# Kernel optimization log

Measured on AMD Instinct MI355X. Metric: run time of the kernel, lower is better.

Reference implementation:

```python
import jax, jax.numpy as jnp
import numpy as np

DEPTH = 4
EPS = 1e-5


def block_pool(x, g):
    # adaptive max pool over a g x g grid of blocks, broadcast back to full size.
    # Equivalent to the recursive HalfSplit/adaptive_max_pool2d/QuarterStitch pyramid.
    B, C, H, W = x.shape
    xr = x.reshape(B, C, g, H // g, g, W // g)
    m = xr.max(axis=(3, 5), keepdims=True)          # [B,C,g,1,g,1]
    return jnp.broadcast_to(m, xr.shape).reshape(B, C, H, W)


def conv1x1_bn(x, w, gamma, beta):
    # Conv2DNormed: 1x1 conv (no bias) followed by BatchNorm (batch statistics).
    y = jnp.einsum('bchw,oc->bohw', x, w)
    mu = y.mean(axis=(0, 2, 3), keepdims=True)
    var = y.var(axis=(0, 2, 3), keepdims=True)
    yhat = (y - mu) * jax.lax.rsqrt(var + EPS)
    return yhat * gamma[None, :, None, None] + beta[None, :, None, None]


def setup_inputs() -> dict:
    key = jax.random.key(0)
    k0, k1, k2 = jax.random.split(key, 3)
    B, C, H, W = 4, 256, 192, 192
    x = jax.random.normal(k0, (B, C, H, W), jnp.float32)
    ws = jax.random.normal(k1, (DEPTH, C, C), jnp.float32) / np.float32(np.sqrt(C))
    gs = jnp.ones((DEPTH, C), jnp.float32)
    bs = jnp.zeros((DEPTH, C), jnp.float32)
    wf = jax.random.normal(k2, (C, (DEPTH + 1) * C), jnp.float32) / np.float32(np.sqrt((DEPTH + 1) * C))
    gf = jnp.ones((C,), jnp.float32)
    bf = jnp.zeros((C,), jnp.float32)
    return {"x": x, "ws": ws, "gs": gs, "bs": bs, "wf": wf, "gf": gf, "bf": bf}


def reference(x, ws, gs, bs, wf, gf, bf):
    # p[0] = raw input; p[1+d] = conv_d(block-pooled input at grid 2^d), d=0..DEPTH-1
    p = [x]
    for d in range(DEPTH):
        pooled = block_pool(x, 2 ** d)
        p.append(conv1x1_bn(pooled, ws[d], gs[d], bs[d]))
    out = jnp.concatenate(p, axis=1)                # [B, (DEPTH+1)*C, H, W]
    return conv1x1_bn(out, wf, gf, bf)
```

## Files before the change

### kernel.cpp

```cpp
#include <hip/hip_runtime.h>

typedef unsigned short u16;
typedef unsigned int   u32;
typedef __attribute__((ext_vector_type(4))) float f32x4;
typedef __attribute__((ext_vector_type(8))) short s16x8;
typedef __attribute__((ext_vector_type(4))) unsigned short u16x4;
typedef __attribute__((ext_vector_type(8))) unsigned short u16x8;

#define HW    36864
#define NCH   256
#define NB    4
#define NPIX  147456
#define POS   85
#define BN_EPS 1e-5f
#define NBKT  16

#define WS_PALL    0
#define WS_YD      87040
#define WS_PSUM    174080
#define WS_PSQ     175104
#define WS_CONTRIB 176128
#define WS_FSUMB   241664
#define WS_FSQB    245760
#define WS_WPK     249856
#define WS_YBF     282624
#define WS_TOT1    (WS_YBF + NB*NCH*HW/2)

__device__ __forceinline__ u16 f2bf(float f) {
  u32 u = __builtin_bit_cast(u32, f);
  u += 0x7fffu + ((u >> 16) & 1u);
  return (u16)(u >> 16);
}
__device__ __forceinline__ float bf2f(u16 h) {
  u32 u = ((u32)h) << 16;
  return __builtin_bit_cast(float, u);
}

__global__ __launch_bounds__(192) void k_pool(const float* __restrict__ x, float* __restrict__ wsb) {
  __shared__ float sm[8][4][48];
  __shared__ float sp[84];
  int bc = blockIdx.x;
  const float* base = x + (size_t)bc * HW;
  int t = threadIdx.x;
  int cg = t % 48, rg = t / 48;
  if (bc == 0) {
    for (int i = t; i < 2048; i += 192) wsb[WS_PSUM + i] = 0.f;
    for (int i = t; i < 8192; i += 192) wsb[WS_FSUMB + i] = 0.f;
  }
  #pragma unroll
  for (int byi = 0; byi < 8; byi++) {
    float mm = -3.4e38f;
    #pragma unroll
    for (int rr = 0; rr < 6; rr++) {
      int r = byi*24 + rg + 4*rr;
      f32x4 v = *(const f32x4*)(base + r*192 + cg*4);
      mm = fmaxf(mm, fmaxf(fmaxf(v.x, v.y), fmaxf(v.z, v.w)));
    }
    sm[byi][rg][cg] = mm;
  }
  __syncthreads();
  size_t pb = WS_PALL + (size_t)bc * POS;
  if (t < 64) {
    int by = t >> 3, bx = t & 7;
    float mm = -3.4e38f;
    for (int r2 = 0; r2 < 4; r2++)
      for (int cq = 0; cq < 6; cq++)
        mm = fmaxf(mm, sm[by][r2][bx*6 + cq]);
    sp[t] = mm;
    wsb[pb + t] = mm;
  }
  __syncthreads();
  if (t < 16) {
    int i = t >> 2, j = t & 3;
    float mm = fmaxf(fmaxf(sp[(2*i)*8 + 2*j], sp[(2*i)*8 + 2*j + 1]),
                     fmaxf(sp[(2*i+1)*8 + 2*j], sp[(2*i+1)*8 + 2*j + 1]));
    sp[64 + t] = mm;
    wsb[pb + 64 + t] = mm;
  }
  __syncthreads();
  if (t < 4) {
    int i = t >> 1, j = t & 1;
    float mm = fmaxf(fmaxf(sp[64 + (2*i)*4 + 2*j], sp[64 + (2*i)*4 + 2*j + 1]),
                     fmaxf(sp[64 + (2*i+1)*4 + 2*j], sp[64 + (2*i+1)*4 + 2*j + 1]));
    sp[80 + t] = mm;
    wsb[pb + 80 + t] = mm;
  }
  __syncthreads();
  if (t == 0)
    wsb[pb + 84] = fmaxf(fmaxf(sp[80], sp[81]), fmaxf(sp[82], sp[83]));
}

__global__ __launch_bounds__(256) void k_wpack(const float* __restrict__ wf, float* __restrict__ wsb) {
  int fid = blockIdx.x*256 + threadIdx.x;
  int m = fid & 255, g = (fid >> 8) & 3, ks = fid >> 10;
  const float* src = wf + (size_t)m*1280 + ks*32 + g*8;
  f32x4 a = *(const f32x4*)src;
  f32x4 c = *(const f32x4*)(src + 4);
  u32* dst = (u32*)((u16*)(wsb + WS_WPK) + (size_t)fid*8);
  dst[0] = (u32)f2bf(a.x) | ((u32)f2bf(a.y) << 16);
  dst[1] = (u32)f2bf(a.z) | ((u32)f2bf(a.w) << 16);
  dst[2] = (u32)f2bf(c.x) | ((u32)f2bf(c.y) << 16);
  dst[3] = (u32)f2bf(c.z) | ((u32)f2bf(c.w) << 16);
}

__global__ __launch_bounds__(256) void k_pyr(const float* __restrict__ wconv, float* __restrict__ wsb) {
  __shared__ __align__(16) float pv[256];
  int bi = blockIdx.x;
  int b = bi / 85, pos = bi % 85;
  int d = (pos < 64) ? 3 : (pos < 80) ? 2 : (pos < 84) ? 1 : 0;
  int t = threadIdx.x;
  pv[t] = wsb[WS_PALL + (size_t)(b*NCH + t)*POS + pos];
  __syncthreads();
  const float* wrow = wconv + ((size_t)d*NCH + t)*NCH;
  float acc = 0.f;
  #pragma unroll 4
  for (int c4 = 0; c4 < 64; c4++) {
    f32x4 wv = *(const f32x4*)(wrow + c4*4);
    f32x4 xv = *(const f32x4*)(&pv[c4*4]);
    acc += wv.x*xv.x + wv.y*xv.y + wv.z*xv.z + wv.w*xv.w;
  }
  wsb[WS_YD + (size_t)(b*NCH + t)*POS + pos] = acc;
  atomicAdd(&wsb[WS_PSUM + d*NCH + t], acc);
  atomicAdd(&wsb[WS_PSQ  + d*NCH + t], acc*acc);
}

__global__ __launch_bounds__(256) void k_contrib(const float* __restrict__ wf,
                                                 const float* __restrict__ gs,
                                                 const float* __restrict__ bs,
                                                 float* __restrict__ wsb) {
  __shared__ __align__(16) float pn[16][256];
  int cell = blockIdx.x;
  int by = cell >> 3, bx = cell & 7;
  int t = threadIdx.x;
  #pragma unroll
  for (int d = 0; d < 4; d++) {
    int pos = (d == 3) ? cell
            : (d == 2) ? 64 + (by >> 1)*4 + (bx >> 1)
            : (d == 1) ? 80 + (by >> 2)*2 + (bx >> 2)
            : 84;
    float cnt = (float)(4 << (2*d));
    float mu  = wsb[WS_PSUM + d*NCH + t] / cnt;
    float var = wsb[WS_PSQ  + d*NCH + t] / cnt - mu*mu;
    float sc  = gs[d*NCH + t] * rsqrtf(var + BN_EPS);
    float bi_ = bs[d*NCH + t] - mu * sc;
    #pragma unroll
    for (int b = 0; b < 4; b++)
      pn[d*4 + b][t] = wsb[WS_YD + (size_t)(b*NCH + t)*POS + pos] * sc + bi_;
  }
  __syncthreads();
  float a0 = 0.f, a1 = 0.f, a2 = 0.f, a3 = 0.f;
  #pragma unroll
  for (int d = 0; d < 4; d++) {
    const float* wrow = wf + (size_t)t*1280 + 256 + d*256;
    #pragma unroll 4
    for (int j = 0; j < 64; j++) {
      f32x4 wv = *(const f32x4*)(wrow + j*4);
      f32x4 p0 = *(const f32x4*)(&pn[d*4 + 0][j*4]);
      f32x4 p1 = *(const f32x4*)(&pn[d*4 + 1][j*4]);
      f32x4 p2 = *(const f32x4*)(&pn[d*4 + 2][j*4]);
      f32x4 p3 = *(const f32x4*)(&pn[d*4 + 3][j*4]);
      a0 += wv.x*p0.x + wv.y*p0.y + wv.z*p0.z + wv.w*p0.w;
      a1 += wv.x*p1.x + wv.y*p1.y + wv.z*p1.z + wv.w*p1.w;
      a2 += wv.x*p2.x + wv.y*p2.y + wv.z*p2.z + wv.w*p2.w;
      a3 += wv.x*p3.x + wv.y*p3.y + wv.z*p3.z + wv.w*p3.w;
    }
  }
  wsb[WS_CONTRIB + (size_t)(0*NCH + t)*64 + cell] = a0;
  wsb[WS_CONTRIB + (size_t)(1*NCH + t)*64 + cell] = a1;
  wsb[WS_CONTRIB + (size_t)(2*NCH + t)*64 + cell] = a2;
  wsb[WS_CONTRIB + (size_t)(3*NCH + t)*64 + cell] = a3;
}

template<bool YBF>
__global__ __launch_bounds__(256, 3) void k_main(const float* __restrict__ x,
                                                 float* __restrict__ wsb, float* __restrict__ y) {
  __shared__ __align__(16) u32 xbuf[2][64*20];
  __shared__ float ctile[256*4];
  __shared__ __align__(16) u16 ytile[256*72];
  int wg = blockIdx.x;
  int b = wg / 576, tile = wg % 576;
  int n0 = tile * 64;
  int t = threadIdx.x, w = t >> 6, l = t & 63, g = l >> 4, ln = l & 15;
  int cb0 = (tile % 3) * 64;
  int rowblk = (tile / 3) / 24;
  int cblk0 = cb0 / 24;
  const u16* wpk = (const u16*)(wsb + WS_WPK);
  int mrow = w*64 + ln;
  int qq = t & 15, c2 = t >> 4;
  const float* xsrc = x + (size_t)(b*NCH + 2*c2)*HW + n0 + 4*qq;

  float ct[4];
  {
    const float* cbase = wsb + WS_CONTRIB + ((size_t)b*NCH + t)*64 + rowblk*8;
    #pragma unroll
    for (int i = 0; i < 4; i++) {
      int cc = cblk0 + i; if (cc > 7) cc = 7;
      ct[i] = cbase[cc];
    }
  }
  f32x4 xa[4], xbv[4];
  #pragma unroll
  for (int i = 0; i < 4; i++) {
    xa[i]  = *(const f32x4*)(xsrc + (size_t)(i*32)*HW);
    xbv[i] = *(const f32x4*)(xsrc + (size_t)(i*32 + 1)*HW);
  }
  s16x8 af[2][4];
  #pragma unroll
  for (int tm = 0; tm < 4; tm++)
    af[0][tm] = *(const s16x8*)(wpk + ((size_t)g*256 + mrow + tm*16)*8);

  #pragma unroll
  for (int i = 0; i < 4; i++) ctile[t*4 + i] = ct[i];
  asm volatile("s_waitcnt lgkmcnt(0)" ::: "memory");
  __builtin_amdgcn_s_barrier();
  __builtin_amdgcn_sched_barrier(0);

  f32x4 acc[4][4];
  #pragma unroll
  for (int i = 0; i < 4; i++)
    #pragma unroll
    for (int j = 0; j < 4; j++)
      acc[i][j] = {0.f, 0.f, 0.f, 0.f};

  int slot = (((c2 >> 2) ^ (qq & 3)) << 2) | (c2 & 3);

  #pragma unroll
  for (int i = 0; i < 8; i++) {
    {
      u32* dst = &xbuf[i & 1][0];
      f32x4 va = xa[i & 3], vb = xbv[i & 3];
      #pragma unroll
      for (int j = 0; j < 4; j++) {
        u32 pk = (u32)f2bf(va[j]) | ((u32)f2bf(vb[j]) << 16);
        dst[(4*qq + j)*20 + slot] = pk;
      }
    }
    asm volatile("s_waitcnt lgkmcnt(0)" ::: "memory");
    __builtin_amdgcn_s_barrier();
    __builtin_amdgcn_sched_barrier(0);
    if (i < 4) {
      xa[i & 3]  = *(const f32x4*)(xsrc + (size_t)((i+4)*32)*HW);
      xbv[i & 3] = *(const f32x4*)(xsrc + (size_t)((i+4)*32 + 1)*HW);
    }
    if (i < 7) {
      #pragma unroll
      for (int tm = 0; tm < 4; tm++)
        af[(i+1) & 1][tm] = *(const s16x8*)(wpk + ((size_t)((i+1)*4 + g)*256 + mrow + tm*16)*8);
    }
    #pragma unroll
    for (int tn = 0; tn < 4; tn++) {
      int px = 16*tn + ln;
      int gr = g ^ ((px >> 2) & 3);
      s16x8 bfr = *(const s16x8*)((const u16*)&xbuf[i & 1][px*20 + gr*4]);
      #pragma unroll
      for (int tm = 0; tm < 4; tm++)
        acc[tm][tn] = __builtin_amdgcn_mfma_f32_16x16x32_bf16(af[i & 1][tm], bfr, acc[tm][tn], 0, 0, 0);
    }
  }

  int ci[4];
  #pragma unroll
  for (int tn = 0; tn < 4; tn++)
    ci[tn] = (cb0 + 16*tn + ln)/24 - cblk0;
  int bkt = wg & (NBKT - 1);
  float* fsum = wsb + WS_FSUMB + bkt*256;
  float* fsq  = wsb + WS_FSQB  + bkt*256;
  float* yf   = y + (size_t)b*NCH*HW + n0;
  #pragma unroll
  for (int tm = 0; tm < 4; tm++) {
    #pragma unroll
    for (int r = 0; r < 4; r++) {
      int o = w*64 + tm*16 + g*4 + r;
      float s1 = 0.f, s2 = 0.f;
      #pragma unroll
      for (int tn = 0; tn < 4; tn++) {
        int px = 16*tn + ln;
        float v = acc[tm][tn][r] + ctile[o*4 + ci[tn]];
        if (YBF) {
          u16 h = f2bf(v);
          ytile[o*72 + px] = h;
          float yr = bf2f(h);
          s1 += yr; s2 += yr*yr;
        } else {
          yf[(size_t)o*HW + px] = v;
          s1 += v; s2 += v*v;
        }
      }
      s1 += __shfl_xor(s1, 1);  s2 += __shfl_xor(s2, 1);
      s1 += __shfl_xor(s1, 2);  s2 += __shfl_xor(s2, 2);
      s1 += __shfl_xor(s1, 4);  s2 += __shfl_xor(s2, 4);
      s1 += __shfl_xor(s1, 8);  s2 += __shfl_xor(s2, 8);
      if (ln == 0) { atomicAdd(&fsum[o], s1); atomicAdd(&fsq[o], s2); }
    }
  }
  if (YBF) {
    __syncthreads();
    u16* ybb = (u16*)(wsb + WS_YBF) + (size_t)b*NCH*HW + n0;
    int oo = t >> 3, seg = t & 7;
    #pragma unroll
    for (int r8 = 0; r8 < 8; r8++) {
      int o = r8*32 + oo;
      u16x8 v = *(const u16x8*)(&ytile[o*72 + seg*8]);
      *(u16x8*)(ybb + (size_t)o*HW + seg*8) = v;
    }
  }
}

template<bool YBF>
__global__ __launch_bounds__(256) void k_norm(float* __restrict__ out,
                                              const float* __restrict__ gf,
                                              const float* __restrict__ bfv,
                                              const float* __restrict__ wsb) {
  int bid = blockIdx.x;
  int plane = bid >> 2, q = bid & 3;
  int c = plane & 255;
  float s1 = 0.f, s2 = 0.f;
  #pragma unroll
  for (int i = 0; i < NBKT; i++) {
    s1 += wsb[WS_FSUMB + i*256 + c];
    s2 += wsb[WS_FSQB  + i*256 + c];
  }
  float inv = 1.f / (float)NPIX;
  float mu  = s1 * inv;
  float var = s2 * inv - mu*mu;
  float sc  = gf[c] * rsqrtf(var + BN_EPS);
  float bi  = bfv[c] - mu * sc;
  size_t base4 = ((size_t)plane*HW + q*(HW/4)) >> 2;
  int t = threadIdx.x;
  if (YBF) {
    const u16* yb = (const u16*)(wsb + WS_YBF);
    #pragma unroll
    for (int it = 0; it < 9; it++) {
      size_t i4 = base4 + it*256 + t;
      u16x4 v = *(const u16x4*)(yb + i4*4);
      f32x4 o;
      o.x = bf2f(v[0])*sc + bi;
      o.y = bf2f(v[1])*sc + bi;
      o.z = bf2f(v[2])*sc + bi;
      o.w = bf2f(v[3])*sc + bi;
      ((f32x4*)out)[i4] = o;
    }
  } else {
    #pragma unroll
    for (int it = 0; it < 9; it++) {
      size_t i4 = base4 + it*256 + t;
      f32x4 v = ((f32x4*)out)[i4];
      v.x = v.x*sc + bi; v.y = v.y*sc + bi; v.z = v.z*sc + bi; v.w = v.w*sc + bi;
      ((f32x4*)out)[i4] = v;
    }
  }
}

extern "C" void kernel_launch(void* const* d_in, const int* in_sizes, int n_in,
                              void* d_out, int out_size, void* d_ws, size_t ws_size,
                              hipStream_t stream) {
  const float* x  = (const float*)d_in[0];
  const float* w  = (const float*)d_in[1];
  const float* gs = (const float*)d_in[2];
  const float* bs = (const float*)d_in[3];
  const float* wf = (const float*)d_in[4];
  const float* gf = (const float*)d_in[5];
  const float* bf = (const float*)d_in[6];
  float* y   = (float*)d_out;
  float* wsb = (float*)d_ws;

  bool ybf = ws_size >= (size_t)WS_TOT1 * sizeof(float);

  k_pool   <<<NB*NCH, 192, 0, stream>>>(x, wsb);
  k_wpack  <<<32, 256, 0, stream>>>(wf, wsb);
  k_pyr    <<<NB*POS, 256, 0, stream>>>(w, wsb);
  k_contrib<<<64, 256, 0, stream>>>(wf, gs, bs, wsb);
  if (ybf) k_main<true> <<<NB*576, 256, 0, stream>>>(x, wsb, y);
  else     k_main<false><<<NB*576, 256, 0, stream>>>(x, wsb, y);
  if (ybf) k_norm<true> <<<4096, 256, 0, stream>>>(y, gf, bf, wsb);
  else     k_norm<false><<<4096, 256, 0, stream>>>(y, gf, bf, wsb);
}
```

Before: 201.8 us.

## Fuse block max-pool into main GEMM and defer per-cell pyramid contribution

Removes the separate pooling pass over x by computing per-cell maxima inside the main GEMM kernel with LDS and global atomicMax on order-preserving float encodings. The pyramid contribution is no longer added before bf16 rounding. Instead, per-cell sums of y are accumulated and the final BN statistics are reconstructed analytically in a new single-block stats kernel, with the per-cell additive term folded into the normalize pass. This saves one full read of x but adds atomics, a serial single-block reduction kernel, and a small change in numerics.

```diff
diff --git a/kernel.cpp b/kernel.cpp
--- a/kernel.cpp
+++ b/kernel.cpp
@@ -15,15 +15,18 @@
 #define BN_EPS 1e-5f
 #define NBKT  16
 
-#define WS_PALL    0
-#define WS_YD      87040
-#define WS_PSUM    174080
-#define WS_PSQ     175104
-#define WS_CONTRIB 176128
-#define WS_FSUMB   241664
-#define WS_FSQB    245760
-#define WS_WPK     249856
-#define WS_YBF     282624
+#define WS_P3      0
+#define WS_PALL    65536
+#define WS_YD      152576
+#define WS_PSUM    239616
+#define WS_PSQ     240640
+#define WS_CONTRIB 241664
+#define WS_S1      307200
+#define WS_FSQB    372736
+#define WS_SC      376832
+#define WS_ADD     377088
+#define WS_WPK     442624
+#define WS_YBF     475392
 #define WS_TOT1    (WS_YBF + NB*NCH*HW/2)
 
 __device__ __forceinline__ u16 f2bf(float f) {
@@ -35,63 +38,26 @@
   u32 u = ((u32)h) << 16;
   return __builtin_bit_cast(float, u);
 }
-
-__global__ __launch_bounds__(192) void k_pool(const float* __restrict__ x, float* __restrict__ wsb) {
-  __shared__ float sm[8][4][48];
-  __shared__ float sp[84];
-  int bc = blockIdx.x;
-  const float* base = x + (size_t)bc * HW;
-  int t = threadIdx.x;
-  int cg = t % 48, rg = t / 48;
-  if (bc == 0) {
-    for (int i = t; i < 2048; i += 192) wsb[WS_PSUM + i] = 0.f;
-    for (int i = t; i < 8192; i += 192) wsb[WS_FSUMB + i] = 0.f;
-  }
-  #pragma unroll
-  for (int byi = 0; byi < 8; byi++) {
-    float mm = -3.4e38f;
-    #pragma unroll
-    for (int rr = 0; rr < 6; rr++) {
-      int r = byi*24 + rg + 4*rr;
-      f32x4 v = *(const f32x4*)(base + r*192 + cg*4);
-      mm = fmaxf(mm, fmaxf(fmaxf(v.x, v.y), fmaxf(v.z, v.w)));
-    }
-    sm[byi][rg][cg] = mm;
-  }
-  __syncthreads();
-  size_t pb = WS_PALL + (size_t)bc * POS;
-  if (t < 64) {
-    int by = t >> 3, bx = t & 7;
-    float mm = -3.4e38f;
-    for (int r2 = 0; r2 < 4; r2++)
-      for (int cq = 0; cq < 6; cq++)
-        mm = fmaxf(mm, sm[by][r2][bx*6 + cq]);
-    sp[t] = mm;
-    wsb[pb + t] = mm;
-  }
-  __syncthreads();
-  if (t < 16) {
-    int i = t >> 2, j = t & 3;
-    float mm = fmaxf(fmaxf(sp[(2*i)*8 + 2*j], sp[(2*i)*8 + 2*j + 1]),
-                     fmaxf(sp[(2*i+1)*8 + 2*j], sp[(2*i+1)*8 + 2*j + 1]));
-    sp[64 + t] = mm;
-    wsb[pb + 64 + t] = mm;
-  }
-  __syncthreads();
-  if (t < 4) {
-    int i = t >> 1, j = t & 1;
-    float mm = fmaxf(fmaxf(sp[64 + (2*i)*4 + 2*j], sp[64 + (2*i)*4 + 2*j + 1]),
-                     fmaxf(sp[64 + (2*i+1)*4 + 2*j], sp[64 + (2*i+1)*4 + 2*j + 1]));
-    sp[80 + t] = mm;
-    wsb[pb + 80 + t] = mm;
-  }
-  __syncthreads();
-  if (t == 0)
-    wsb[pb + 84] = fmaxf(fmaxf(sp[80], sp[81]), fmaxf(sp[82], sp[83]));
+__device__ __forceinline__ u32 encf(float f) {
+  u32 b = __builtin_bit_cast(u32, f);
+  return (b & 0x80000000u) ? ~b : (b | 0x80000000u);
+}
+__device__ __forceinline__ float decf(u32 k) {
+  u32 b = (k & 0x80000000u) ? (k & 0x7fffffffu) : ~k;
+  return __builtin_bit_cast(float, b);
 }
 
 __global__ __launch_bounds__(256) void k_wpack(const float* __restrict__ wf, float* __restrict__ wsb) {
-  int fid = blockIdx.x*256 + threadIdx.x;
+  int blk = blockIdx.x, t = threadIdx.x;
+  if (blk >= 32) {
+    int id = (blk - 32)*256 + t;
+    wsb[WS_P3 + id] = 0.f;
+    wsb[WS_S1 + id] = 0.f;
+    if (id < 4096) wsb[WS_FSQB + id] = 0.f;
+    if (id < 2048) wsb[WS_PSUM + id] = 0.f;
+    return;
+  }
+  int fid = blk*256 + t;
   int m = fid & 255, g = (fid >> 8) & 3, ks = fid >> 10;
   const float* src = wf + (size_t)m*1280 + ks*32 + g*8;
   f32x4 a = *(const f32x4*)src;
@@ -101,6 +67,216 @@
   dst[1] = (u32)f2bf(a.z) | ((u32)f2bf(a.w) << 16);
   dst[2] = (u32)f2bf(c.x) | ((u32)f2bf(c.y) << 16);
   dst[3] = (u32)f2bf(c.z) | ((u32)f2bf(c.w) << 16);
+}
+
+template<bool YBF>
+__global__ __launch_bounds__(256, 3) void k_main(const float* __restrict__ x,
+                                                 float* __restrict__ wsb, float* __restrict__ y) {
+  __shared__ __align__(16) u32 xbuf[2][64*20];
+  __shared__ u32 pmaxl[256*4];
+  __shared__ __align__(16) u16 ytile[128*72];
+  int wg = blockIdx.x;
+  int b = wg / 576, tile = wg % 576;
+  int n0 = tile * 64;
+  int row = tile / 3;
+  int t = threadIdx.x, w = t >> 6, l = t & 63, g = l >> 4, ln = l & 15;
+  int cb0 = (tile % 3) * 64;
+  int cblk0 = cb0 / 24;
+  int maxcl = (cb0 + 63)/24 - cblk0;
+  int cellbase = (row/24)*8 + cblk0;
+  const u16* wpk = (const u16*)(wsb + WS_WPK);
+  int mrow = w*64 + ln;
+  int qq = t & 15, c2 = t >> 4;
+  int cellLoc = (cb0 + 4*qq)/24 - cblk0;
+  const float* xsrc = x + (size_t)(b*NCH + 2*c2)*HW + n0 + 4*qq;
+
+  #pragma unroll
+  for (int j = 0; j < 4; j++) pmaxl[t*4 + j] = 0u;
+
+  f32x4 xa[4], xbv[4];
+  #pragma unroll
+  for (int i = 0; i < 4; i++) {
+    xa[i]  = *(const f32x4*)(xsrc + (size_t)(i*32)*HW);
+    xbv[i] = *(const f32x4*)(xsrc + (size_t)(i*32 + 1)*HW);
+  }
+  s16x8 af[2][4];
+  #pragma unroll
+  for (int tm = 0; tm < 4; tm++)
+    af[0][tm] = *(const s16x8*)(wpk + ((size_t)g*256 + mrow + tm*16)*8);
+
+  asm volatile("s_waitcnt lgkmcnt(0)" ::: "memory");
+  __builtin_amdgcn_s_barrier();
+  __builtin_amdgcn_sched_barrier(0);
+
+  f32x4 acc[4][4];
+  #pragma unroll
+  for (int i = 0; i < 4; i++)
+    #pragma unroll
+    for (int j = 0; j < 4; j++)
+      acc[i][j] = {0.f, 0.f, 0.f, 0.f};
+
+  int slot = (((c2 >> 2) ^ (qq & 3)) << 2) | (c2 & 3);
+
+  #pragma unroll
+  for (int i = 0; i < 8; i++) {
+    {
+      u32* dst = &xbuf[i & 1][0];
+      f32x4 va = xa[i & 3], vb = xbv[i & 3];
+      #pragma unroll
+      for (int j = 0; j < 4; j++) {
+        u32 pk = (u32)f2bf(va[j]) | ((u32)f2bf(vb[j]) << 16);
+        dst[(4*qq + j)*20 + slot] = pk;
+      }
+      float ma = fmaxf(fmaxf(va.x, va.y), fmaxf(va.z, va.w));
+      float mb = fmaxf(fmaxf(vb.x, vb.y), fmaxf(vb.z, vb.w));
+      int ca = 2*c2 + 32*i;
+      atomicMax(&pmaxl[ca*4 + cellLoc], encf(ma));
+      atomicMax(&pmaxl[(ca + 1)*4 + cellLoc], encf(mb));
+    }
+    asm volatile("s_waitcnt lgkmcnt(0)" ::: "memory");
+    __builtin_amdgcn_s_barrier();
+    __builtin_amdgcn_sched_barrier(0);
+    if (i < 4) {
+      xa[i & 3]  = *(const f32x4*)(xsrc + (size_t)((i+4)*32)*HW);
+      xbv[i & 3] = *(const f32x4*)(xsrc + (size_t)((i+4)*32 + 1)*HW);
+    }
+    if (i < 7) {
+      #pragma unroll
+      for (int tm = 0; tm < 4; tm++)
+        af[(i+1) & 1][tm] = *(const s16x8*)(wpk + ((size_t)((i+1)*4 + g)*256 + mrow + tm*16)*8);
+    }
+    #pragma unroll
+    for (int tn = 0; tn < 4; tn++) {
+      int px = 16*tn + ln;
+      int gr = g ^ ((px >> 2) & 3);
+      s16x8 bfr = *(const s16x8*)((const u16*)&xbuf[i & 1][px*20 + gr*4]);
+      #pragma unroll
+      for (int tm = 0; tm < 4; tm++)
+        acc[tm][tn] = __builtin_amdgcn_mfma_f32_16x16x32_bf16(af[i & 1][tm], bfr, acc[tm][tn], 0, 0, 0);
+    }
+  }
+
+  {
+    u32* P3g = (u32*)(wsb + WS_P3) + ((size_t)(b*NCH + t))*64 + cellbase;
+    #pragma unroll
+    for (int j = 0; j < 4; j++) {
+      if (j <= maxcl) { u32 v = pmaxl[t*4 + j]; if (v) atomicMax(&P3g[j], v); }
+    }
+  }
+
+  int bkt = wg & (NBKT - 1);
+  float* fsqb = wsb + WS_FSQB + bkt*256;
+  float* S1g  = wsb + WS_S1 + ((size_t)b*NCH)*64;
+
+  if (YBF) {
+    u16* ybb = (u16*)(wsb + WS_YBF) + (size_t)b*NCH*HW + n0;
+    #pragma unroll
+    for (int half = 0; half < 2; half++) {
+      if ((w >> 1) == half) {
+        #pragma unroll
+        for (int tm = 0; tm < 4; tm++)
+          #pragma unroll
+          for (int r = 0; r < 4; r++) {
+            int orow = (w & 1)*64 + tm*16 + g*4 + r;
+            #pragma unroll
+            for (int tn = 0; tn < 4; tn++)
+              ytile[orow*72 + 16*tn + ln] = f2bf(acc[tm][tn][r]);
+          }
+      }
+      __syncthreads();
+      int oo = t >> 3, seg = t & 7;
+      int basec = cb0 + seg*8;
+      int loG = basec/24, hiG = (basec + 7)/24;
+      int kk = (loG + 1)*24 - basec; if (kk > 8) kk = 8;
+      int lo = loG - cblk0, hi = hiG - cblk0;
+      #pragma unroll
+      for (int r8 = 0; r8 < 4; r8++) {
+        int ol = r8*32 + oo;
+        int o  = half*128 + ol;
+        u16x8 v = *(const u16x8*)&ytile[ol*72 + seg*8];
+        *(u16x8*)(ybb + (size_t)o*HW + seg*8) = v;
+        float p_lo = 0.f, p_hi = 0.f, s2p = 0.f;
+        #pragma unroll
+        for (int e = 0; e < 8; e++) {
+          float yr = bf2f(v[e]);
+          s2p += yr*yr;
+          if (e < kk) p_lo += yr; else p_hi += yr;
+        }
+        s2p += __shfl_xor(s2p, 1); s2p += __shfl_xor(s2p, 2); s2p += __shfl_xor(s2p, 4);
+        if (seg == 0) atomicAdd(&fsqb[o], s2p);
+        float* S1o = S1g + (size_t)o*64 + cellbase;
+        #pragma unroll
+        for (int cl = 0; cl < 4; cl++) {
+          float val = (lo == cl ? p_lo : 0.f) + (hi == cl ? p_hi : 0.f);
+          val += __shfl_xor(val, 1); val += __shfl_xor(val, 2); val += __shfl_xor(val, 4);
+          if (seg == cl && cl <= maxcl) atomicAdd(&S1o[cl], val);
+        }
+      }
+      __syncthreads();
+    }
+  } else {
+    float* yf = y + (size_t)b*NCH*HW + n0;
+    #pragma unroll
+    for (int tm = 0; tm < 4; tm++) {
+      #pragma unroll
+      for (int r = 0; r < 4; r++) {
+        int o = w*64 + tm*16 + g*4 + r;
+        float s1c0 = 0.f, s1c1 = 0.f, s1c2 = 0.f, s1c3 = 0.f, s2 = 0.f;
+        #pragma unroll
+        for (int tn = 0; tn < 4; tn++) {
+          int px = 16*tn + ln;
+          float v = acc[tm][tn][r];
+          yf[(size_t)o*HW + px] = v;
+          int ci = (cb0 + px)/24 - cblk0;
+          s1c0 += (ci == 0) ? v : 0.f;
+          s1c1 += (ci == 1) ? v : 0.f;
+          s1c2 += (ci == 2) ? v : 0.f;
+          s1c3 += (ci == 3) ? v : 0.f;
+          s2 += v*v;
+        }
+        s2 += __shfl_xor(s2, 1); s2 += __shfl_xor(s2, 2);
+        s2 += __shfl_xor(s2, 4); s2 += __shfl_xor(s2, 8);
+        if (ln == 0) atomicAdd(&fsqb[o], s2);
+        float* S1o = S1g + (size_t)o*64 + cellbase;
+        float sv[4] = {s1c0, s1c1, s1c2, s1c3};
+        #pragma unroll
+        for (int cl = 0; cl < 4; cl++) {
+          float val = sv[cl];
+          val += __shfl_xor(val, 1); val += __shfl_xor(val, 2);
+          val += __shfl_xor(val, 4); val += __shfl_xor(val, 8);
+          if (ln == cl && cl <= maxcl) atomicAdd(&S1o[cl], val);
+        }
+      }
+    }
+  }
+}
+
+__global__ __launch_bounds__(64) void k_ppyr(float* __restrict__ wsb) {
+  __shared__ float sm3[64], sm2[16], sm1[4];
+  int bc = blockIdx.x;
+  int t = threadIdx.x;
+  const u32* p3 = (const u32*)(wsb + WS_P3) + (size_t)bc*64;
+  float leaf = decf(p3[t]);
+  sm3[t] = leaf;
+  __syncthreads();
+  float* pb = wsb + WS_PALL + (size_t)bc*POS;
+  pb[t] = leaf;
+  if (t < 16) {
+    int i = t >> 2, j = t & 3;
+    float m = fmaxf(fmaxf(sm3[(2*i)*8 + 2*j], sm3[(2*i)*8 + 2*j + 1]),
+                    fmaxf(sm3[(2*i+1)*8 + 2*j], sm3[(2*i+1)*8 + 2*j + 1]));
+    sm2[t] = m; pb[64 + t] = m;
+  }
+  __syncthreads();
+  if (t < 4) {
+    int i = t >> 1, j = t & 1;
+    float m = fmaxf(fmaxf(sm2[(2*i)*4 + 2*j], sm2[(2*i)*4 + 2*j + 1]),
+                    fmaxf(sm2[(2*i+1)*4 + 2*j], sm2[(2*i+1)*4 + 2*j + 1]));
+    sm1[t] = m; pb[80 + t] = m;
+  }
+  __syncthreads();
+  if (t == 0)
+    pb[84] = fmaxf(fmaxf(sm1[0], sm1[1]), fmaxf(sm1[2], sm1[3]));
 }
 
 __global__ __launch_bounds__(256) void k_pyr(const float* __restrict__ wconv, float* __restrict__ wsb) {
@@ -171,181 +347,75 @@
   wsb[WS_CONTRIB + (size_t)(3*NCH + t)*64 + cell] = a3;
 }
 
-template<bool YBF>
-__global__ __launch_bounds__(256, 3) void k_main(const float* __restrict__ x,
-                                                 float* __restrict__ wsb, float* __restrict__ y) {
-  __shared__ __align__(16) u32 xbuf[2][64*20];
-  __shared__ float ctile[256*4];
-  __shared__ __align__(16) u16 ytile[256*72];
-  int wg = blockIdx.x;
-  int b = wg / 576, tile = wg % 576;
-  int n0 = tile * 64;
-  int t = threadIdx.x, w = t >> 6, l = t & 63, g = l >> 4, ln = l & 15;
-  int cb0 = (tile % 3) * 64;
-  int rowblk = (tile / 3) / 24;
-  int cblk0 = cb0 / 24;
-  const u16* wpk = (const u16*)(wsb + WS_WPK);
-  int mrow = w*64 + ln;
-  int qq = t & 15, c2 = t >> 4;
-  const float* xsrc = x + (size_t)(b*NCH + 2*c2)*HW + n0 + 4*qq;
-
-  float ct[4];
-  {
-    const float* cbase = wsb + WS_CONTRIB + ((size_t)b*NCH + t)*64 + rowblk*8;
-    #pragma unroll
-    for (int i = 0; i < 4; i++) {
-      int cc = cblk0 + i; if (cc > 7) cc = 7;
-      ct[i] = cbase[cc];
-    }
-  }
-  f32x4 xa[4], xbv[4];
-  #pragma unroll
-  for (int i = 0; i < 4; i++) {
-    xa[i]  = *(const f32x4*)(xsrc + (size_t)(i*32)*HW);
-    xbv[i] = *(const f32x4*)(xsrc + (size_t)(i*32 + 1)*HW);
-  }
-  s16x8 af[2][4];
-  #pragma unroll
-  for (int tm = 0; tm < 4; tm++)
-    af[0][tm] = *(const s16x8*)(wpk + ((size_t)g*256 + mrow + tm*16)*8);
-
-  #pragma unroll
-  for (int i = 0; i < 4; i++) ctile[t*4 + i] = ct[i];
-  asm volatile("s_waitcnt lgkmcnt(0)" ::: "memory");
-  __builtin_amdgcn_s_barrier();
-  __builtin_amdgcn_sched_barrier(0);
-
-  f32x4 acc[4][4];
-  #pragma unroll
-  for (int i = 0; i < 4; i++)
-    #pragma unroll
-    for (int j = 0; j < 4; j++)
-      acc[i][j] = {0.f, 0.f, 0.f, 0.f};
-
-  int slot = (((c2 >> 2) ^ (qq & 3)) << 2) | (c2 & 3);
-
-  #pragma unroll
-  for (int i = 0; i < 8; i++) {
-    {
-      u32* dst = &xbuf[i & 1][0];
-      f32x4 va = xa[i & 3], vb = xbv[i & 3];
-      #pragma unroll
-      for (int j = 0; j < 4; j++) {
-        u32 pk = (u32)f2bf(va[j]) | ((u32)f2bf(vb[j]) << 16);
-        dst[(4*qq + j)*20 + slot] = pk;
-      }
-    }
-    asm volatile("s_waitcnt lgkmcnt(0)" ::: "memory");
-    __builtin_amdgcn_s_barrier();
-    __builtin_amdgcn_sched_barrier(0);
-    if (i < 4) {
-      xa[i & 3]  = *(const f32x4*)(xsrc + (size_t)((i+4)*32)*HW);
-      xbv[i & 3] = *(const f32x4*)(xsrc + (size_t)((i+4)*32 + 1)*HW);
-    }
-    if (i < 7) {
-      #pragma unroll
-      for (int tm = 0; tm < 4; tm++)
-        af[(i+1) & 1][tm] = *(const s16x8*)(wpk + ((size_t)((i+1)*4 + g)*256 + mrow + tm*16)*8);
-    }
-    #pragma unroll
-    for (int tn = 0; tn < 4; tn++) {
-      int px = 16*tn + ln;
-      int gr = g ^ ((px >> 2) & 3);
-      s16x8 bfr = *(const s16x8*)((const u16*)&xbuf[i & 1][px*20 + gr*4]);
-      #pragma unroll
-      for (int tm = 0; tm < 4; tm++)
-        acc[tm][tn] = __builtin_amdgcn_mfma_f32_16x16x32_bf16(af[i & 1][tm], bfr, acc[tm][tn], 0, 0, 0);
-    }
-  }
-
-  int ci[4];
-  #pragma unroll
-  for (int tn = 0; tn < 4; tn++)
-    ci[tn] = (cb0 + 16*tn + ln)/24 - cblk0;
-  int bkt = wg & (NBKT - 1);
-  float* fsum = wsb + WS_FSUMB + bkt*256;
-  float* fsq  = wsb + WS_FSQB  + bkt*256;
-  float* yf   = y + (size_t)b*NCH*HW + n0;
-  #pragma unroll
-  for (int tm = 0; tm < 4; tm++) {
-    #pragma unroll
-    for (int r = 0; r < 4; r++) {
-      int o = w*64 + tm*16 + g*4 + r;
-      float s1 = 0.f, s2 = 0.f;
-      #pragma unroll
-      for (int tn = 0; tn < 4; tn++) {
-        int px = 16*tn + ln;
-        float v = acc[tm][tn][r] + ctile[o*4 + ci[tn]];
-        if (YBF) {
-          u16 h = f2bf(v);
-          ytile[o*72 + px] = h;
-          float yr = bf2f(h);
-          s1 += yr; s2 += yr*yr;
-        } else {
-          yf[(size_t)o*HW + px] = v;
-          s1 += v; s2 += v*v;
-        }
-      }
-      s1 += __shfl_xor(s1, 1);  s2 += __shfl_xor(s2, 1);
-      s1 += __shfl_xor(s1, 2);  s2 += __shfl_xor(s2, 2);
-      s1 += __shfl_xor(s1, 4);  s2 += __shfl_xor(s2, 4);
-      s1 += __shfl_xor(s1, 8);  s2 += __shfl_xor(s2, 8);
-      if (ln == 0) { atomicAdd(&fsum[o], s1); atomicAdd(&fsq[o], s2); }
-    }
-  }
-  if (YBF) {
-    __syncthreads();
-    u16* ybb = (u16*)(wsb + WS_YBF) + (size_t)b*NCH*HW + n0;
-    int oo = t >> 3, seg = t & 7;
-    #pragma unroll
-    for (int r8 = 0; r8 < 8; r8++) {
-      int o = r8*32 + oo;
-      u16x8 v = *(const u16x8*)(&ytile[o*72 + seg*8]);
-      *(u16x8*)(ybb + (size_t)o*HW + seg*8) = v;
-    }
+__global__ __launch_bounds__(256) void k_fstats(const float* __restrict__ gf,
+                                                const float* __restrict__ bfv,
+                                                float* __restrict__ wsb) {
+  int o = threadIdx.x;
+  float sq = 0.f;
+  #pragma unroll
+  for (int i = 0; i < NBKT; i++) sq += wsb[WS_FSQB + i*256 + o];
+  float sum1 = 0.f, sum2 = sq;
+  #pragma unroll 8
+  for (int bc = 0; bc < 256; bc++) {
+    int b = bc >> 6, cell = bc & 63;
+    float s1 = wsb[WS_S1      + ((size_t)(b*NCH + o))*64 + cell];
+    float c  = wsb[WS_CONTRIB + ((size_t)(b*NCH + o))*64 + cell];
+    sum1 += s1 + 576.f*c;
+    sum2 += c*(2.f*s1 + 576.f*c);
+  }
+  float inv = 1.f / (float)NPIX;
+  float mu  = sum1 * inv;
+  float var = sum2 * inv - mu*mu;
+  float sc  = gf[o] * rsqrtf(var + BN_EPS);
+  float bi  = bfv[o] - mu * sc;
+  wsb[WS_SC + o] = sc;
+  #pragma unroll 8
+  for (int bc = 0; bc < 256; bc++) {
+    int b = bc >> 6, cell = bc & 63;
+    float c = wsb[WS_CONTRIB + ((size_t)(b*NCH + o))*64 + cell];
+    wsb[WS_ADD + ((size_t)(b*NCH + o))*64 + cell] = bi + c*sc;
   }
 }
 
 template<bool YBF>
 __global__ __launch_bounds__(256) void k_norm(float* __restrict__ out,
-                                              const float* __restrict__ gf,
-                                              const float* __restrict__ bfv,
                                               const float* __restrict__ wsb) {
+  __shared__ float a16[16];
   int bid = blockIdx.x;
   int plane = bid >> 2, q = bid & 3;
-  int c = plane & 255;
-  float s1 = 0.f, s2 = 0.f;
-  #pragma unroll
-  for (int i = 0; i < NBKT; i++) {
-    s1 += wsb[WS_FSUMB + i*256 + c];
-    s2 += wsb[WS_FSQB  + i*256 + c];
-  }
-  float inv = 1.f / (float)NPIX;
-  float mu  = s1 * inv;
-  float var = s2 * inv - mu*mu;
-  float sc  = gf[c] * rsqrtf(var + BN_EPS);
-  float bi  = bfv[c] - mu * sc;
+  int t = threadIdx.x;
+  float sc = wsb[WS_SC + (plane & 255)];
+  if (t < 16)
+    a16[t] = wsb[WS_ADD + (size_t)plane*64 + (2*q + (t >> 3))*8 + (t & 7)];
+  __syncthreads();
   size_t base4 = ((size_t)plane*HW + q*(HW/4)) >> 2;
-  int t = threadIdx.x;
   if (YBF) {
     const u16* yb = (const u16*)(wsb + WS_YBF);
     #pragma unroll
     for (int it = 0; it < 9; it++) {
+      int pl = 4*(it*256 + t);
+      int rl = pl / 192;
+      int cc = (pl - rl*192) / 24;
+      float ad = a16[(rl/24)*8 + cc];
       size_t i4 = base4 + it*256 + t;
       u16x4 v = *(const u16x4*)(yb + i4*4);
       f32x4 o;
-      o.x = bf2f(v[0])*sc + bi;
-      o.y = bf2f(v[1])*sc + bi;
-      o.z = bf2f(v[2])*sc + bi;
-      o.w = bf2f(v[3])*sc + bi;
+      o.x = bf2f(v[0])*sc + ad;
+      o.y = bf2f(v[1])*sc + ad;
+      o.z = bf2f(v[2])*sc + ad;
+      o.w = bf2f(v[3])*sc + ad;
       ((f32x4*)out)[i4] = o;
     }
   } else {
     #pragma unroll
     for (int it = 0; it < 9; it++) {
+      int pl = 4*(it*256 + t);
+      int rl = pl / 192;
+      int cc = (pl - rl*192) / 24;
+      float ad = a16[(rl/24)*8 + cc];
       size_t i4 = base4 + it*256 + t;
       f32x4 v = ((f32x4*)out)[i4];
-      v.x = v.x*sc + bi; v.y = v.y*sc + bi; v.z = v.z*sc + bi; v.w = v.w*sc + bi;
+      v.x = v.x*sc + ad; v.y = v.y*sc + ad; v.z = v.z*sc + ad; v.w = v.w*sc + ad;
       ((f32x4*)out)[i4] = v;
     }
   }
@@ -366,12 +436,13 @@
 
   bool ybf = ws_size >= (size_t)WS_TOT1 * sizeof(float);
 
-  k_pool   <<<NB*NCH, 192, 0, stream>>>(x, wsb);
-  k_wpack  <<<32, 256, 0, stream>>>(wf, wsb);
+  k_wpack  <<<288, 256, 0, stream>>>(wf, wsb);
+  if (ybf) k_main<true> <<<NB*576, 256, 0, stream>>>(x, wsb, y);
+  else     k_main<false><<<NB*576, 256, 0, stream>>>(x, wsb, y);
+  k_ppyr   <<<NB*NCH, 64, 0, stream>>>(wsb);
   k_pyr    <<<NB*POS, 256, 0, stream>>>(w, wsb);
   k_contrib<<<64, 256, 0, stream>>>(wf, gs, bs, wsb);
-  if (ybf) k_main<true> <<<NB*576, 256, 0, stream>>>(x, wsb, y);
-  else     k_main<false><<<NB*576, 256, 0, stream>>>(x, wsb, y);
-  if (ybf) k_norm<true> <<<4096, 256, 0, stream>>>(y, gf, bf, wsb);
-  else     k_norm<false><<<4096, 256, 0, stream>>>(y, gf, bf, wsb);
-}
+  k_fstats <<<1, 256, 0, stream>>>(gf, bf, wsb);
+  if (ybf) k_norm<true> <<<4096, 256, 0, stream>>>(y, wsb);
+  else     k_norm<false><<<4096, 256, 0, stream>>>(y, wsb);
+}
```

New measurement: 354.2 us. 75.5% more time.

## Fold weight packing into pool kernel and double K-step per barrier in main GEMM

Applied to the files above, without the earlier changes.

Merges the bf16 weight-packing kernel into the pooling kernel as extra blocks, removing one launch. In the main GEMM kernel, each barrier phase now stages two 32-channel K slices into LDS instead of one, which halves the barrier count. The xbuf and ytile buffers now share one LDS allocation, separated by a __syncthreads, to reduce shared memory per block. Weight fragments are loaded just before use instead of being prefetched one step ahead, so their global-load latency may be exposed.

```diff
diff --git a/kernel.cpp b/kernel.cpp
--- a/kernel.cpp
+++ b/kernel.cpp
@@ -36,12 +36,30 @@
   return __builtin_bit_cast(float, u);
 }
 
-__global__ __launch_bounds__(192) void k_pool(const float* __restrict__ x, float* __restrict__ wsb) {
+__global__ __launch_bounds__(192) void k_pool(const float* __restrict__ x,
+                                              const float* __restrict__ wf,
+                                              float* __restrict__ wsb) {
+  int blk = blockIdx.x;
+  int t = threadIdx.x;
+  if (blk >= 1024) {
+    int fid = (blk - 1024)*192 + t;
+    if (fid < 8192) {
+      int m = fid & 255, g = (fid >> 8) & 3, ks = fid >> 10;
+      const float* src = wf + (size_t)m*1280 + ks*32 + g*8;
+      f32x4 a = *(const f32x4*)src;
+      f32x4 c = *(const f32x4*)(src + 4);
+      u32* dst = (u32*)((u16*)(wsb + WS_WPK) + (size_t)fid*8);
+      dst[0] = (u32)f2bf(a.x) | ((u32)f2bf(a.y) << 16);
+      dst[1] = (u32)f2bf(a.z) | ((u32)f2bf(a.w) << 16);
+      dst[2] = (u32)f2bf(c.x) | ((u32)f2bf(c.y) << 16);
+      dst[3] = (u32)f2bf(c.z) | ((u32)f2bf(c.w) << 16);
+    }
+    return;
+  }
   __shared__ float sm[8][4][48];
   __shared__ float sp[84];
-  int bc = blockIdx.x;
+  int bc = blk;
   const float* base = x + (size_t)bc * HW;
-  int t = threadIdx.x;
   int cg = t % 48, rg = t / 48;
   if (bc == 0) {
     for (int i = t; i < 2048; i += 192) wsb[WS_PSUM + i] = 0.f;
@@ -88,19 +106,6 @@
   __syncthreads();
   if (t == 0)
     wsb[pb + 84] = fmaxf(fmaxf(sp[80], sp[81]), fmaxf(sp[82], sp[83]));
-}
-
-__global__ __launch_bounds__(256) void k_wpack(const float* __restrict__ wf, float* __restrict__ wsb) {
-  int fid = blockIdx.x*256 + threadIdx.x;
-  int m = fid & 255, g = (fid >> 8) & 3, ks = fid >> 10;
-  const float* src = wf + (size_t)m*1280 + ks*32 + g*8;
-  f32x4 a = *(const f32x4*)src;
-  f32x4 c = *(const f32x4*)(src + 4);
-  u32* dst = (u32*)((u16*)(wsb + WS_WPK) + (size_t)fid*8);
-  dst[0] = (u32)f2bf(a.x) | ((u32)f2bf(a.y) << 16);
-  dst[1] = (u32)f2bf(a.z) | ((u32)f2bf(a.w) << 16);
-  dst[2] = (u32)f2bf(c.x) | ((u32)f2bf(c.y) << 16);
-  dst[3] = (u32)f2bf(c.z) | ((u32)f2bf(c.w) << 16);
 }
 
 __global__ __launch_bounds__(256) void k_pyr(const float* __restrict__ wconv, float* __restrict__ wsb) {
@@ -174,9 +179,9 @@
 template<bool YBF>
 __global__ __launch_bounds__(256, 3) void k_main(const float* __restrict__ x,
                                                  float* __restrict__ wsb, float* __restrict__ y) {
-  __shared__ __align__(16) u32 xbuf[2][64*20];
+  __shared__ __align__(16) char smem[40960];
   __shared__ float ctile[256*4];
-  __shared__ __align__(16) u16 ytile[256*72];
+  u32* xbuf = (u32*)smem;
   int wg = blockIdx.x;
   int b = wg / 576, tile = wg % 576;
   int n0 = tile * 64;
@@ -198,22 +203,19 @@
       ct[i] = cbase[cc];
     }
   }
-  f32x4 xa[4], xbv[4];
-  #pragma unroll
-  for (int i = 0; i < 4; i++) {
-    xa[i]  = *(const f32x4*)(xsrc + (size_t)(i*32)*HW);
-    xbv[i] = *(const f32x4*)(xsrc + (size_t)(i*32 + 1)*HW);
-  }
-  s16x8 af[2][4];
-  #pragma unroll
-  for (int tm = 0; tm < 4; tm++)
-    af[0][tm] = *(const s16x8*)(wpk + ((size_t)g*256 + mrow + tm*16)*8);
+  f32x4 xr[2][2][2];
+  #pragma unroll
+  for (int pp = 0; pp < 2; pp++)
+    #pragma unroll
+    for (int s = 0; s < 2; s++)
+      #pragma unroll
+      for (int h = 0; h < 2; h++)
+        xr[pp][s][h] = *(const f32x4*)(xsrc + (size_t)((pp*2 + s)*32 + h)*HW);
 
   #pragma unroll
   for (int i = 0; i < 4; i++) ctile[t*4 + i] = ct[i];
   asm volatile("s_waitcnt lgkmcnt(0)" ::: "memory");
   __builtin_amdgcn_s_barrier();
-  __builtin_amdgcn_sched_barrier(0);
 
   f32x4 acc[4][4];
   #pragma unroll
@@ -225,39 +227,50 @@
   int slot = (((c2 >> 2) ^ (qq & 3)) << 2) | (c2 & 3);
 
   #pragma unroll
-  for (int i = 0; i < 8; i++) {
+  for (int p = 0; p < 4; p++) {
     {
-      u32* dst = &xbuf[i & 1][0];
-      f32x4 va = xa[i & 3], vb = xbv[i & 3];
-      #pragma unroll
-      for (int j = 0; j < 4; j++) {
-        u32 pk = (u32)f2bf(va[j]) | ((u32)f2bf(vb[j]) << 16);
-        dst[(4*qq + j)*20 + slot] = pk;
+      u32* dst = xbuf + (p & 1)*2560;
+      #pragma unroll
+      for (int s = 0; s < 2; s++) {
+        f32x4 va = xr[p & 1][s][0], vb = xr[p & 1][s][1];
+        #pragma unroll
+        for (int j = 0; j < 4; j++) {
+          u32 pk = (u32)f2bf(va[j]) | ((u32)f2bf(vb[j]) << 16);
+          dst[(4*qq + j)*40 + s*20 + slot] = pk;
+        }
       }
     }
     asm volatile("s_waitcnt lgkmcnt(0)" ::: "memory");
     __builtin_amdgcn_s_barrier();
-    __builtin_amdgcn_sched_barrier(0);
-    if (i < 4) {
-      xa[i & 3]  = *(const f32x4*)(xsrc + (size_t)((i+4)*32)*HW);
-      xbv[i & 3] = *(const f32x4*)(xsrc + (size_t)((i+4)*32 + 1)*HW);
-    }
-    if (i < 7) {
+    if (p < 2) {
+      #pragma unroll
+      for (int s = 0; s < 2; s++)
+        #pragma unroll
+        for (int h = 0; h < 2; h++)
+          xr[p & 1][s][h] = *(const f32x4*)(xsrc + (size_t)(((p+2)*2 + s)*32 + h)*HW);
+    }
+    #pragma unroll
+    for (int s = 0; s < 2; s++) {
+      int sl = p*2 + s;
+      s16x8 af[4];
       #pragma unroll
       for (int tm = 0; tm < 4; tm++)
-        af[(i+1) & 1][tm] = *(const s16x8*)(wpk + ((size_t)((i+1)*4 + g)*256 + mrow + tm*16)*8);
-    }
-    #pragma unroll
-    for (int tn = 0; tn < 4; tn++) {
-      int px = 16*tn + ln;
-      int gr = g ^ ((px >> 2) & 3);
-      s16x8 bfr = *(const s16x8*)((const u16*)&xbuf[i & 1][px*20 + gr*4]);
-      #pragma unroll
-      for (int tm = 0; tm < 4; tm++)
-        acc[tm][tn] = __builtin_amdgcn_mfma_f32_16x16x32_bf16(af[i & 1][tm], bfr, acc[tm][tn], 0, 0, 0);
-    }
-  }
-
+        af[tm] = *(const s16x8*)(wpk + ((size_t)(sl*4 + g)*256 + mrow + tm*16)*8);
+      const u32* xb = xbuf + (p & 1)*2560 + s*20;
+      #pragma unroll
+      for (int tn = 0; tn < 4; tn++) {
+        int px = 16*tn + ln;
+        int gr = g ^ ((px >> 2) & 3);
+        s16x8 bfr = *(const s16x8*)((const u16*)&xb[px*40 + gr*4]);
+        #pragma unroll
+        for (int tm = 0; tm < 4; tm++)
+          acc[tm][tn] = __builtin_amdgcn_mfma_f32_16x16x32_bf16(af[tm], bfr, acc[tm][tn], 0, 0, 0);
+      }
+    }
+  }
+
+  __syncthreads();
+  u16* ytile = (u16*)smem;
   int ci[4];
   #pragma unroll
   for (int tn = 0; tn < 4; tn++)
@@ -366,8 +379,7 @@
 
   bool ybf = ws_size >= (size_t)WS_TOT1 * sizeof(float);
 
-  k_pool   <<<NB*NCH, 192, 0, stream>>>(x, wsb);
-  k_wpack  <<<32, 256, 0, stream>>>(wf, wsb);
+  k_pool   <<<1068, 192, 0, stream>>>(x, wf, wsb);
   k_pyr    <<<NB*POS, 256, 0, stream>>>(w, wsb);
   k_contrib<<<64, 256, 0, stream>>>(wf, gs, bs, wsb);
   if (ybf) k_main<true> <<<NB*576, 256, 0, stream>>>(x, wsb, y);
```

New measurement: 198.5 us. About the same (-1.7%).
